# Performance work log

Measured on AMD Instinct MI355X. Metric: run time of the kernel, lower is better.

## Reference

```python
import jax, jax.numpy as jnp
import numpy as np

B = 256        # number of trees
L0 = 4096      # leaves per tree
L1 = 256       # layer-1 nodes per tree
D = 128        # input_dim == hidden_dim
OUT = 32       # output classes
EPS = 1e-5
N0 = B * L0    # 1,048,576 total leaves
N1 = B * L1    # 65,536 layer-1 nodes
N2 = B         # one root per tree


def _bn(x, g, b):
    # training-mode BatchNorm1d: biased variance over the node axis
    m = jnp.mean(x, axis=0)
    v = jnp.mean((x - m) ** 2, axis=0)
    return g * (x - m) * jax.lax.rsqrt(v + EPS) + b


def _mlp(h, w1, b1, g, beta, w2, b2):
    # GIN-style 2-layer MLP: relu(bn(linear)) -> linear
    return jax.nn.relu(_bn(h @ w1 + b1, g, beta)) @ w2 + b2


def setup_inputs() -> dict:
    key = jax.random.key(0)
    ks = jax.random.split(key, 16)

    def lin(k, fin, fout):
        kw, kb = jax.random.split(k)
        s = 1.0 / np.sqrt(fin)
        return (jax.random.uniform(kw, (fin, fout), jnp.float32, -s, s),
                jax.random.uniform(kb, (fout,), jnp.float32, -s, s))

    x = jax.random.normal(ks[0], (N0, D), jnp.float32)
    # structured tree indices: contiguous children per parent, contiguous trees
    parent1 = jnp.arange(N0, dtype=jnp.int64) // (L0 // L1)   # leaf -> layer1 parent (global)
    parent2 = jnp.arange(N1, dtype=jnp.int64) // L1           # layer1 -> root (global)
    tree0 = jnp.arange(N0, dtype=jnp.int64) // L0             # leaf -> tree id
    tree1 = jnp.arange(N1, dtype=jnp.int64) // L1             # layer1 node -> tree id

    m1w1, m1b1 = lin(ks[1], D, D)
    m1w2, m1b2 = lin(ks[2], D, D)
    m2w1, m2b1 = lin(ks[3], D, D)
    m2w2, m2b2 = lin(ks[4], D, D)
    wp, bp = lin(ks[5], D + 2 * D, OUT)

    ones = jnp.ones((D,), jnp.float32)
    zeros = jnp.zeros((D,), jnp.float32)
    return {
        "x": x, "parent1": parent1, "parent2": parent2, "tree0": tree0, "tree1": tree1,
        "mlp1_w1": m1w1, "mlp1_b1": m1b1, "mlp1_g": ones, "mlp1_beta": zeros,
        "mlp1_w2": m1w2, "mlp1_b2": m1b2, "bn1_g": ones, "bn1_b": zeros,
        "mlp2_w1": m2w1, "mlp2_b1": m2b1, "mlp2_g": ones, "mlp2_beta": zeros,
        "mlp2_w2": m2w2, "mlp2_b2": m2b2, "bn2_g": ones, "bn2_b": zeros,
        "wp": wp, "bp": bp,
    }


def reference(x, parent1, parent2, tree0, tree1,
              mlp1_w1, mlp1_b1, mlp1_g, mlp1_beta, mlp1_w2, mlp1_b2, bn1_g, bn1_b,
              mlp2_w1, mlp2_b1, mlp2_g, mlp2_beta, mlp2_w2, mlp2_b2, bn2_g, bn2_b,
              wp, bp):
    # layer 1: sparse child-sum (spmm with all-ones tree adjacency == segment_sum)
    p1 = jax.ops.segment_sum(x, parent1, num_segments=N1)              # [N1, D]
    h1 = jax.nn.relu(_bn(_mlp(p1, mlp1_w1, mlp1_b1, mlp1_g, mlp1_beta, mlp1_w2, mlp1_b2), bn1_g, bn1_b))
    # layer 2 (roots)
    p2 = jax.ops.segment_sum(h1, parent2, num_segments=N2)             # [B, D]
    h2 = jax.nn.relu(_bn(_mlp(p2, mlp2_w1, mlp2_b1, mlp2_g, mlp2_beta, mlp2_w2, mlp2_b2), bn2_g, bn2_b))
    # tree sum-pooling of layers 0..depth-1; layer depth is already per-tree
    g0 = jax.ops.segment_sum(x, tree0, num_segments=B)                 # [B, D]
    g1 = jax.ops.segment_sum(h1, tree1, num_segments=B)                # [B, D]
    rep = jnp.concatenate([g0, g1, h2], axis=1)                        # [B, 3D]
    return jax.nn.softmax(rep @ wp + bp, axis=1)                       # [B, OUT]
```

## Files before the change

### kernel.cpp

```cpp
#include <hip/hip_runtime.h>
#include <math.h>

#define D      128
#define D4     32
#define NTREE  256
#define NL1    65536
#define EPSBN  1e-5f

#define SC_OFF 0L
#define SD_OFF 256L
#define G0_OFF 512L
#define P2_OFF 33280L
#define ZERO_CNT 66048
#define SA_OFF 66048L
#define SB_OFF 66304L
#define T2_OFF 66560L
#define PBA_OFF 99328L
#define PBB_OFF 361472L
#define T1_OFF 623616L
#define U_OFF  9012224L

#define FMA4(A_, S_, W_) { (A_).x = fmaf((S_),(W_).x,(A_).x); (A_).y = fmaf((S_),(W_).y,(A_).y); \
                           (A_).z = fmaf((S_),(W_).z,(A_).z); (A_).w = fmaf((S_),(W_).w,(A_).w); }
#define ADD4(A_, B_)     { (A_).x += (B_).x; (A_).y += (B_).y; (A_).z += (B_).z; (A_).w += (B_).w; }
#define SQ4(Q_, V_)      { (Q_).x = fmaf((V_).x,(V_).x,(Q_).x); (Q_).y = fmaf((V_).y,(V_).y,(Q_).y); \
                           (Q_).z = fmaf((V_).z,(V_).z,(Q_).z); (Q_).w = fmaf((V_).w,(V_).w,(Q_).w); }
#define F4Z              make_float4(0.f,0.f,0.f,0.f)

__global__ __launch_bounds__(256) void k_zero(float* __restrict__ ws) {
    int i = blockIdx.x * 256 + threadIdx.x;
    if (i < ZERO_CNT) ws[i] = 0.f;
}

__global__ __launch_bounds__(256) void k_fused1(const float* __restrict__ x,
        const float* __restrict__ w1, const float* __restrict__ b1,
        float* __restrict__ t1, float* __restrict__ g0, float* __restrict__ pbufA)
{
    __shared__ __align__(16) float tile[64][D];
    __shared__ __align__(16) float red[2][8][D];
    const int t = threadIdx.x, b = blockIdx.x;
    const int w  = t >> 6;
    const int ln = t & 63;
    const int lc = ln & 31;
    const float4* __restrict__ x4 = (const float4*)x;

    float4 gacc = F4Z;
    #pragma unroll
    for (int pp = 0; pp < 4; ++pp) {
        const int p0 = pp * 16 + w * 4;
        #pragma unroll
        for (int r = 0; r < 4; ++r) {
            const long prow = (long)b * 64 + p0 + r;
            const long base = prow * 512 + ln;
            float4 a = F4Z;
            #pragma unroll
            for (int j = 0; j < 8; ++j) {
                float4 v = x4[base + j * 64];
                ADD4(a, v)
            }
            float4 o;
            o.x = __shfl_xor(a.x, 32); o.y = __shfl_xor(a.y, 32);
            o.z = __shfl_xor(a.z, 32); o.w = __shfl_xor(a.w, 32);
            ADD4(a, o)
            if (ln < 32) {
                *(float4*)&tile[p0 + r][lc*4] = a;
                ADD4(gacc, a)
            }
        }
    }
    if (ln < 32) *(float4*)&red[0][w][lc*4] = gacc;
    __syncthreads();
    if (t < 32) {
        float4 G = F4Z;
        #pragma unroll
        for (int g = 0; g < 4; ++g) { float4 vg = *(const float4*)&red[0][g][t*4]; ADD4(G, vg) }
        const int tree = b >> 2;
        atomicAdd(&g0[tree*D + t*4+0], G.x); atomicAdd(&g0[tree*D + t*4+1], G.y);
        atomicAdd(&g0[tree*D + t*4+2], G.z); atomicAdd(&g0[tree*D + t*4+3], G.w);
    }

    const int tc = t & 31, rg = t >> 5;
    float4* __restrict__ tv = (float4*)t1;
    const long base = (long)b * 64;
    float4 acc[8];
    const float4 bb = ((const float4*)b1)[tc];
    #pragma unroll
    for (int r = 0; r < 8; ++r) acc[r] = bb;
    const float4* __restrict__ wv = (const float4*)w1;
    #pragma unroll 4
    for (int k4 = 0; k4 < 32; ++k4) {
        float4 wr0 = wv[(k4*4+0)*D4 + tc];
        float4 wr1 = wv[(k4*4+1)*D4 + tc];
        float4 wr2 = wv[(k4*4+2)*D4 + tc];
        float4 wr3 = wv[(k4*4+3)*D4 + tc];
        #pragma unroll
        for (int r = 0; r < 8; ++r) {
            float4 a4 = *(const float4*)&tile[rg*8 + r][k4*4];
            FMA4(acc[r], a4.x, wr0) FMA4(acc[r], a4.y, wr1)
            FMA4(acc[r], a4.z, wr2) FMA4(acc[r], a4.w, wr3)
        }
    }
    #pragma unroll
    for (int r = 0; r < 8; ++r) tv[(base + rg*8 + r) * D4 + tc] = acc[r];

    float4 s4 = F4Z, q4 = F4Z;
    #pragma unroll
    for (int r = 0; r < 8; ++r) { ADD4(s4, acc[r]) SQ4(q4, acc[r]) }
    __syncthreads();
    *(float4*)&red[0][rg][tc*4] = s4;
    *(float4*)&red[1][rg][tc*4] = q4;
    __syncthreads();
    if (t < 32) {
        float4 S = F4Z;
        #pragma unroll
        for (int g = 0; g < 8; ++g) { float4 vs = *(const float4*)&red[0][g][t*4]; ADD4(S, vs) }
        *(float4*)&pbufA[b*256 + t*4] = S;
    } else if (t < 64) {
        const int c = t - 32;
        float4 Q = F4Z;
        #pragma unroll
        for (int g = 0; g < 8; ++g) { float4 vq = *(const float4*)&red[1][g][c*4]; ADD4(Q, vq) }
        *(float4*)&pbufA[b*256 + 128 + c*4] = Q;
    }
}

__global__ __launch_bounds__(256) void k_statR(const float* __restrict__ pbuf,
                                               float* __restrict__ stats)
{
    __shared__ float red[8][32];
    const int t = threadIdx.x, b = blockIdx.x;
    const int c = b * 32 + (t & 31);
    const int g = t >> 5;
    float s = 0.f;
    #pragma unroll 8
    for (int r = g; r < 1024; r += 8) s += pbuf[r*256 + c];
    red[g][t & 31] = s;
    __syncthreads();
    if (t < 32) {
        float S = 0.f;
        #pragma unroll
        for (int gg = 0; gg < 8; ++gg) S += red[gg][t];
        stats[b*32 + t] = S;
    }
}

__global__ __launch_bounds__(256) void k_mm2(const float* __restrict__ t1,
        const float* __restrict__ w2, const float* __restrict__ b2,
        const float* __restrict__ mg, const float* __restrict__ mbe,
        const float* __restrict__ statsA, float* __restrict__ u,
        float* __restrict__ pbufB)
{
    __shared__ __align__(16) float tile[64][D];
    __shared__ __align__(16) float red[2][8][D];
    const int t = threadIdx.x, b = blockIdx.x;
    const int tc = t & 31, rg = t >> 5;
    const float4* __restrict__ tv = (const float4*)t1;
    float4* __restrict__ uv = (float4*)u;
    const long base = (long)b * 64;

    float4 scv, shv;
    {
        const float inv = 1.f / (float)NL1;
        #pragma unroll
        for (int i = 0; i < 4; ++i) {
            const int c = tc*4 + i;
            float m  = statsA[c] * inv;
            float vv = statsA[D + c] * inv - m * m;
            float rs = rsqrtf(vv + EPSBN);
            float sc = mg[c] * rs;
            ((float*)&scv)[i] = sc;
            ((float*)&shv)[i] = mbe[c] - m * sc;
        }
    }
    #pragma unroll
    for (int i = 0; i < 8; ++i) {
        const int row = i * 8 + rg;
        float4 v = tv[(base + row) * D4 + tc];
        float4 y;
        y.x = fmaxf(fmaf(v.x, scv.x, shv.x), 0.f);
        y.y = fmaxf(fmaf(v.y, scv.y, shv.y), 0.f);
        y.z = fmaxf(fmaf(v.z, scv.z, shv.z), 0.f);
        y.w = fmaxf(fmaf(v.w, scv.w, shv.w), 0.f);
        *(float4*)&tile[row][tc*4] = y;
    }
    __syncthreads();

    float4 acc[8];
    const float4 bb = ((const float4*)b2)[tc];
    #pragma unroll
    for (int r = 0; r < 8; ++r) acc[r] = bb;
    const float4* __restrict__ wv = (const float4*)w2;
    #pragma unroll 4
    for (int k4 = 0; k4 < 32; ++k4) {
        float4 wr0 = wv[(k4*4+0)*D4 + tc];
        float4 wr1 = wv[(k4*4+1)*D4 + tc];
        float4 wr2 = wv[(k4*4+2)*D4 + tc];
        float4 wr3 = wv[(k4*4+3)*D4 + tc];
        #pragma unroll
        for (int r = 0; r < 8; ++r) {
            float4 a4 = *(const float4*)&tile[rg*8 + r][k4*4];
            FMA4(acc[r], a4.x, wr0) FMA4(acc[r], a4.y, wr1)
            FMA4(acc[r], a4.z, wr2) FMA4(acc[r], a4.w, wr3)
        }
    }
    #pragma unroll
    for (int r = 0; r < 8; ++r) uv[(base + rg*8 + r) * D4 + tc] = acc[r];

    float4 s4 = F4Z, q4 = F4Z;
    #pragma unroll
    for (int r = 0; r < 8; ++r) { ADD4(s4, acc[r]) SQ4(q4, acc[r]) }
    __syncthreads();
    *(float4*)&red[0][rg][tc*4] = s4;
    *(float4*)&red[1][rg][tc*4] = q4;
    __syncthreads();
    if (t < 32) {
        float4 S = F4Z;
        #pragma unroll
        for (int g = 0; g < 8; ++g) { float4 vs = *(const float4*)&red[0][g][t*4]; ADD4(S, vs) }
        *(float4*)&pbufB[b*256 + t*4] = S;
    } else if (t < 64) {
        const int c = t - 32;
        float4 Q = F4Z;
        #pragma unroll
        for (int g = 0; g < 8; ++g) { float4 vq = *(const float4*)&red[1][g][c*4]; ADD4(Q, vq) }
        *(float4*)&pbufB[b*256 + 128 + c*4] = Q;
    }
}

__global__ __launch_bounds__(256) void k_pool(const float* __restrict__ u,
        const float* __restrict__ bg, const float* __restrict__ bb_,
        const float* __restrict__ statsB, float* __restrict__ p2)
{
    __shared__ __align__(16) float red[8][D];
    const int t = threadIdx.x, b = blockIdx.x;
    const int tree = b >> 3, chunk = b & 7;
    const int tc = t & 31, rr = t >> 5;
    const float4* __restrict__ uv = (const float4*)u;

    float4 scv, shv;
    {
        const float inv = 1.f / (float)NL1;
        #pragma unroll
        for (int i = 0; i < 4; ++i) {
            const int c = tc*4 + i;
            float m  = statsB[c] * inv;
            float vv = statsB[D + c] * inv - m * m;
            float rs = rsqrtf(vv + EPSBN);
            float sc = bg[c] * rs;
            ((float*)&scv)[i] = sc;
            ((float*)&shv)[i] = bb_[c] - m * sc;
        }
    }
    const long rbase = (long)tree * 256 + chunk * 32;
    float4 ps = F4Z;
    #pragma unroll
    for (int i = 0; i < 4; ++i) {
        const int row = i * 8 + rr;
        float4 v = uv[(rbase + row) * D4 + tc];
        ps.x += fmaxf(fmaf(v.x, scv.x, shv.x), 0.f);
        ps.y += fmaxf(fmaf(v.y, scv.y, shv.y), 0.f);
        ps.z += fmaxf(fmaf(v.z, scv.z, shv.z), 0.f);
        ps.w += fmaxf(fmaf(v.w, scv.w, shv.w), 0.f);
    }
    *(float4*)&red[rr][tc*4] = ps;
    __syncthreads();
    if (t < 32) {
        float4 S = F4Z;
        #pragma unroll
        for (int g = 0; g < 8; ++g) { float4 vs = *(const float4*)&red[g][t*4]; ADD4(S, vs) }
        atomicAdd(&p2[tree*D + t*4+0], S.x); atomicAdd(&p2[tree*D + t*4+1], S.y);
        atomicAdd(&p2[tree*D + t*4+2], S.z); atomicAdd(&p2[tree*D + t*4+3], S.w);
    }
}

__global__ __launch_bounds__(256) void k_root1(const float* __restrict__ p2,
        const float* __restrict__ w1, const float* __restrict__ b1,
        float* __restrict__ t2, float* __restrict__ statsC)
{
    __shared__ __align__(16) float ps[8][D];
    __shared__ __align__(16) float red[2][8][D];
    const int t = threadIdx.x, b = blockIdx.x;
    const int j4 = t & 31, rr = t >> 5;
    *(float4*)&ps[rr][j4*4] = ((const float4*)p2)[(b*8 + rr)*D4 + j4];
    __syncthreads();
    const int row = t >> 5, tc = t & 31;
    const float4* wv = (const float4*)w1;
    float4 acc = ((const float4*)b1)[tc];
    #pragma unroll 8
    for (int k4 = 0; k4 < 32; ++k4) {
        float4 a = *(const float4*)&ps[row][k4*4];
        float4 wr0 = wv[(k4*4+0)*D4 + tc];
        float4 wr1 = wv[(k4*4+1)*D4 + tc];
        float4 wr2 = wv[(k4*4+2)*D4 + tc];
        float4 wr3 = wv[(k4*4+3)*D4 + tc];
        FMA4(acc, a.x, wr0) FMA4(acc, a.y, wr1) FMA4(acc, a.z, wr2) FMA4(acc, a.w, wr3)
    }
    ((float4*)t2)[(b*8 + row)*D4 + tc] = acc;
    float4 q;
    q.x = acc.x*acc.x; q.y = acc.y*acc.y; q.z = acc.z*acc.z; q.w = acc.w*acc.w;
    *(float4*)&red[0][row][tc*4] = acc;
    *(float4*)&red[1][row][tc*4] = q;
    __syncthreads();
    if (t < D) {
        float S = 0.f, Q = 0.f;
        #pragma unroll
        for (int g = 0; g < 8; ++g) { S += red[0][g][t]; Q += red[1][g][t]; }
        atomicAdd(&statsC[t], S);
        atomicAdd(&statsC[D+t], Q);
    }
}

__global__ __launch_bounds__(256) void k_root2(float* __restrict__ t2,
        const float* __restrict__ mg, const float* __restrict__ mb,
        const float* __restrict__ statsC,
        const float* __restrict__ w2, const float* __restrict__ b2,
        float* __restrict__ statsD)
{
    __shared__ __align__(16) float ysr[8][D];
    __shared__ __align__(16) float red[2][8][D];
    __shared__ __align__(16) float scs[D], shs[D];
    const int t = threadIdx.x, b = blockIdx.x;
    if (t < D) {
        float m = statsC[t] * (1.f / 256.f);
        float v = statsC[D+t] * (1.f / 256.f) - m * m;
        float rs = rsqrtf(v + EPSBN);
        float sc = mg[t] * rs;
        scs[t] = sc;
        shs[t] = mb[t] - m * sc;
    }
    __syncthreads();
    const int j4 = t & 31, rr = t >> 5;
    {
        float4 uu = ((const float4*)t2)[(b*8 + rr)*D4 + j4];
        float4 sc4 = *(const float4*)&scs[j4*4];
        float4 sh4 = *(const float4*)&shs[j4*4];
        float4 y;
        y.x = fmaxf(fmaf(uu.x, sc4.x, sh4.x), 0.f);
        y.y = fmaxf(fmaf(uu.y, sc4.y, sh4.y), 0.f);
        y.z = fmaxf(fmaf(uu.z, sc4.z, sh4.z), 0.f);
        y.w = fmaxf(fmaf(uu.w, sc4.w, sh4.w), 0.f);
        *(float4*)&ysr[rr][j4*4] = y;
    }
    __syncthreads();
    const int row = t >> 5, tc = t & 31;
    const float4* wv = (const float4*)w2;
    float4 acc = ((const float4*)b2)[tc];
    #pragma unroll 8
    for (int k4 = 0; k4 < 32; ++k4) {
        float4 a = *(const float4*)&ysr[row][k4*4];
        float4 wr0 = wv[(k4*4+0)*D4 + tc];
        float4 wr1 = wv[(k4*4+1)*D4 + tc];
        float4 wr2 = wv[(k4*4+2)*D4 + tc];
        float4 wr3 = wv[(k4*4+3)*D4 + tc];
        FMA4(acc, a.x, wr0) FMA4(acc, a.y, wr1) FMA4(acc, a.z, wr2) FMA4(acc, a.w, wr3)
    }
    ((float4*)t2)[(b*8 + row)*D4 + tc] = acc;
    float4 q;
    q.x = acc.x*acc.x; q.y = acc.y*acc.y; q.z = acc.z*acc.z; q.w = acc.w*acc.w;
    *(float4*)&red[0][row][tc*4] = acc;
    *(float4*)&red[1][row][tc*4] = q;
    __syncthreads();
    if (t < D) {
        float S = 0.f, Q = 0.f;
        #pragma unroll
        for (int g = 0; g < 8; ++g) { S += red[0][g][t]; Q += red[1][g][t]; }
        atomicAdd(&statsD[t], S);
        atomicAdd(&statsD[D+t], Q);
    }
}

__global__ __launch_bounds__(128) void k_final(const float* __restrict__ u2,
        const float* __restrict__ statsD,
        const float* __restrict__ bg, const float* __restrict__ bb_,
        const float* __restrict__ g0, const float* __restrict__ p2,
        const float* __restrict__ wp, const float* __restrict__ bp,
        float* __restrict__ out)
{
    __shared__ __align__(16) float reps[3*D];
    const int t = threadIdx.x, tree = blockIdx.x;
    if (t < D) {
        float m = statsD[t] * (1.f / 256.f);
        float v = statsD[D+t] * (1.f / 256.f) - m * m;
        float rs = rsqrtf(v + EPSBN);
        float sc = bg[t] * rs;
        float sh = bb_[t] - m * sc;
        reps[2*D + t] = fmaxf(fmaf(u2[tree*D + t], sc, sh), 0.f);
        reps[t]       = g0[tree*D + t];
        reps[D + t]   = p2[tree*D + t];
    }
    __syncthreads();
    if (t < 32) {
        float acc = bp[t];
        #pragma unroll 8
        for (int j = 0; j < 3*D; ++j) acc = fmaf(reps[j], wp[j*32 + t], acc);
        float mx = acc;
        #pragma unroll
        for (int mk = 16; mk > 0; mk >>= 1) mx = fmaxf(mx, __shfl_xor(mx, mk));
        float e = expf(acc - mx);
        float s = e;
        #pragma unroll
        for (int mk = 16; mk > 0; mk >>= 1) s += __shfl_xor(s, mk);
        out[tree*32 + t] = e / s;
    }
}

extern "C" void kernel_launch(void* const* d_in, const int* in_sizes, int n_in,
                              void* d_out, int out_size, void* d_ws, size_t ws_size,
                              hipStream_t stream)
{
    const float* x    = (const float*)d_in[0];
    const float* m1w1 = (const float*)d_in[5];
    const float* m1b1 = (const float*)d_in[6];
    const float* m1g  = (const float*)d_in[7];
    const float* m1be = (const float*)d_in[8];
    const float* m1w2 = (const float*)d_in[9];
    const float* m1b2 = (const float*)d_in[10];
    const float* bn1g = (const float*)d_in[11];
    const float* bn1b = (const float*)d_in[12];
    const float* m2w1 = (const float*)d_in[13];
    const float* m2b1 = (const float*)d_in[14];
    const float* m2g  = (const float*)d_in[15];
    const float* m2be = (const float*)d_in[16];
    const float* m2w2 = (const float*)d_in[17];
    const float* m2b2 = (const float*)d_in[18];
    const float* bn2g = (const float*)d_in[19];
    const float* bn2b = (const float*)d_in[20];
    const float* wp   = (const float*)d_in[21];
    const float* bp   = (const float*)d_in[22];
    float* out = (float*)d_out;
    float* ws  = (float*)d_ws;

    float* sC  = ws + SC_OFF;
    float* sD  = ws + SD_OFF;
    float* g0  = ws + G0_OFF;
    float* p2  = ws + P2_OFF;
    float* sA  = ws + SA_OFF;
    float* sB  = ws + SB_OFF;
    float* t2  = ws + T2_OFF;
    float* pbA = ws + PBA_OFF;
    float* pbB = ws + PBB_OFF;
    float* t1  = ws + T1_OFF;
    float* u   = ws + U_OFF;

    hipLaunchKernelGGL(k_zero,   dim3(258),  dim3(256), 0, stream, ws);
    hipLaunchKernelGGL(k_fused1, dim3(1024), dim3(256), 0, stream, x, m1w1, m1b1, t1, g0, pbA);
    hipLaunchKernelGGL(k_statR,  dim3(8),    dim3(256), 0, stream, pbA, sA);
    hipLaunchKernelGGL(k_mm2,    dim3(1024), dim3(256), 0, stream, t1, m1w2, m1b2, m1g, m1be, sA, u, pbB);
    hipLaunchKernelGGL(k_statR,  dim3(8),    dim3(256), 0, stream, pbB, sB);
    hipLaunchKernelGGL(k_pool,   dim3(2048), dim3(256), 0, stream, u, bn1g, bn1b, sB, p2);
    hipLaunchKernelGGL(k_root1,  dim3(32),   dim3(256), 0, stream, p2, m2w1, m2b1, t2, sC);
    hipLaunchKernelGGL(k_root2,  dim3(32),   dim3(256), 0, stream, t2, m2g, m2be, sC, m2w2, m2b2, sD);
    hipLaunchKernelGGL(k_final,  dim3(256),  dim3(128), 0, stream, t2, sD, bn2g, bn2b, g0, p2, wp, bp, out);
}
```

Baseline: 246.2 us.

## Replace global atomics and zeroing kernel with deterministic partial-buffer reductions

```diff
diff --git a/kernel.cpp b/kernel.cpp
--- a/kernel.cpp
+++ b/kernel.cpp
@@ -7,18 +7,18 @@
 #define NL1    65536
 #define EPSBN  1e-5f
 
-#define SC_OFF 0L
-#define SD_OFF 256L
-#define G0_OFF 512L
-#define P2_OFF 33280L
-#define ZERO_CNT 66048
-#define SA_OFF 66048L
-#define SB_OFF 66304L
-#define T2_OFF 66560L
-#define PBA_OFF 99328L
-#define PBB_OFF 361472L
-#define T1_OFF 623616L
-#define U_OFF  9012224L
+#define SA_OFF   0L
+#define SB_OFF   256L
+#define G0_OFF   512L
+#define P2_OFF   33280L
+#define T2_OFF   66048L
+#define SCP_OFF  98816L
+#define SDP_OFF  107008L
+#define PBP_OFF  115200L
+#define PBA_OFF  377344L
+#define PBB_OFF  1163776L
+#define T1_OFF   1425920L
+#define U_OFF    9814528L
 
 #define FMA4(A_, S_, W_) { (A_).x = fmaf((S_),(W_).x,(A_).x); (A_).y = fmaf((S_),(W_).y,(A_).y); \
                            (A_).z = fmaf((S_),(W_).z,(A_).z); (A_).w = fmaf((S_),(W_).w,(A_).w); }
@@ -27,17 +27,11 @@
                            (Q_).z = fmaf((V_).z,(V_).z,(Q_).z); (Q_).w = fmaf((V_).w,(V_).w,(Q_).w); }
 #define F4Z              make_float4(0.f,0.f,0.f,0.f)
 
-__global__ __launch_bounds__(256) void k_zero(float* __restrict__ ws) {
-    int i = blockIdx.x * 256 + threadIdx.x;
-    if (i < ZERO_CNT) ws[i] = 0.f;
-}
-
 __global__ __launch_bounds__(256) void k_fused1(const float* __restrict__ x,
         const float* __restrict__ w1, const float* __restrict__ b1,
-        float* __restrict__ t1, float* __restrict__ g0, float* __restrict__ pbufA)
+        float* __restrict__ t1, float* __restrict__ pbufA)
 {
     __shared__ __align__(16) float tile[64][D];
-    __shared__ __align__(16) float red[2][8][D];
     const int t = threadIdx.x, b = blockIdx.x;
     const int w  = t >> 6;
     const int ln = t & 63;
@@ -68,16 +62,8 @@
             }
         }
     }
-    if (ln < 32) *(float4*)&red[0][w][lc*4] = gacc;
-    __syncthreads();
-    if (t < 32) {
-        float4 G = F4Z;
-        #pragma unroll
-        for (int g = 0; g < 4; ++g) { float4 vg = *(const float4*)&red[0][g][t*4]; ADD4(G, vg) }
-        const int tree = b >> 2;
-        atomicAdd(&g0[tree*D + t*4+0], G.x); atomicAdd(&g0[tree*D + t*4+1], G.y);
-        atomicAdd(&g0[tree*D + t*4+2], G.z); atomicAdd(&g0[tree*D + t*4+3], G.w);
-    }
+    if (ln < 32) *(float4*)&pbufA[(long)b*768 + 256 + w*128 + lc*4] = gacc;
+    __syncthreads();
 
     const int tc = t & 31, rg = t >> 5;
     float4* __restrict__ tv = (float4*)t1;
@@ -107,6 +93,7 @@
     #pragma unroll
     for (int r = 0; r < 8; ++r) { ADD4(s4, acc[r]) SQ4(q4, acc[r]) }
     __syncthreads();
+    float (*red)[8][D] = (float(*)[8][D])tile;
     *(float4*)&red[0][rg][tc*4] = s4;
     *(float4*)&red[1][rg][tc*4] = q4;
     __syncthreads();
@@ -114,18 +101,51 @@
         float4 S = F4Z;
         #pragma unroll
         for (int g = 0; g < 8; ++g) { float4 vs = *(const float4*)&red[0][g][t*4]; ADD4(S, vs) }
-        *(float4*)&pbufA[b*256 + t*4] = S;
+        *(float4*)&pbufA[(long)b*768 + t*4] = S;
     } else if (t < 64) {
         const int c = t - 32;
         float4 Q = F4Z;
         #pragma unroll
         for (int g = 0; g < 8; ++g) { float4 vq = *(const float4*)&red[1][g][c*4]; ADD4(Q, vq) }
-        *(float4*)&pbufA[b*256 + 128 + c*4] = Q;
-    }
-}
-
-__global__ __launch_bounds__(256) void k_statR(const float* __restrict__ pbuf,
-                                               float* __restrict__ stats)
+        *(float4*)&pbufA[(long)b*768 + 128 + c*4] = Q;
+    }
+}
+
+__global__ __launch_bounds__(256) void k_redA(const float* __restrict__ pbufA,
+        float* __restrict__ statsA, float* __restrict__ g0)
+{
+    const int t = threadIdx.x, b = blockIdx.x;
+    if (b < 8) {
+        __shared__ float red[8][32];
+        const int c = b * 32 + (t & 31);
+        const int g = t >> 5;
+        float s = 0.f;
+        #pragma unroll 8
+        for (int r = g; r < 1024; r += 8) s += pbufA[(long)r*768 + c];
+        red[g][t & 31] = s;
+        __syncthreads();
+        if (t < 32) {
+            float S = 0.f;
+            #pragma unroll
+            for (int gg = 0; gg < 8; ++gg) S += red[gg][t];
+            statsA[b*32 + t] = S;
+        }
+    } else {
+        const int idx = b - 8;
+        const int tree = idx * 2 + (t >> 7);
+        const int c = t & 127;
+        float s = 0.f;
+        #pragma unroll
+        for (int jb = 0; jb < 4; ++jb)
+            #pragma unroll
+            for (int wvi = 0; wvi < 4; ++wvi)
+                s += pbufA[(long)(tree*4 + jb)*768 + 256 + wvi*128 + c];
+        g0[tree*D + c] = s;
+    }
+}
+
+__global__ __launch_bounds__(256) void k_redB(const float* __restrict__ pbuf,
+                                              float* __restrict__ stats)
 {
     __shared__ float red[8][32];
     const int t = threadIdx.x, b = blockIdx.x;
@@ -151,7 +171,6 @@
         float* __restrict__ pbufB)
 {
     __shared__ __align__(16) float tile[64][D];
-    __shared__ __align__(16) float red[2][8][D];
     const int t = threadIdx.x, b = blockIdx.x;
     const int tc = t & 31, rg = t >> 5;
     const float4* __restrict__ tv = (const float4*)t1;
@@ -210,6 +229,7 @@
     #pragma unroll
     for (int r = 0; r < 8; ++r) { ADD4(s4, acc[r]) SQ4(q4, acc[r]) }
     __syncthreads();
+    float (*red)[8][D] = (float(*)[8][D])tile;
     *(float4*)&red[0][rg][tc*4] = s4;
     *(float4*)&red[1][rg][tc*4] = q4;
     __syncthreads();
@@ -229,7 +249,7 @@
 
 __global__ __launch_bounds__(256) void k_pool(const float* __restrict__ u,
         const float* __restrict__ bg, const float* __restrict__ bb_,
-        const float* __restrict__ statsB, float* __restrict__ p2)
+        const float* __restrict__ statsB, float* __restrict__ pbufP)
 {
     __shared__ __align__(16) float red[8][D];
     const int t = threadIdx.x, b = blockIdx.x;
@@ -268,20 +288,29 @@
         float4 S = F4Z;
         #pragma unroll
         for (int g = 0; g < 8; ++g) { float4 vs = *(const float4*)&red[g][t*4]; ADD4(S, vs) }
-        atomicAdd(&p2[tree*D + t*4+0], S.x); atomicAdd(&p2[tree*D + t*4+1], S.y);
-        atomicAdd(&p2[tree*D + t*4+2], S.z); atomicAdd(&p2[tree*D + t*4+3], S.w);
-    }
-}
-
-__global__ __launch_bounds__(256) void k_root1(const float* __restrict__ p2,
+        *(float4*)&pbufP[(long)b*D + t*4] = S;
+    }
+}
+
+__global__ __launch_bounds__(256) void k_root1(const float* __restrict__ pbufP,
         const float* __restrict__ w1, const float* __restrict__ b1,
-        float* __restrict__ t2, float* __restrict__ statsC)
+        float* __restrict__ p2, float* __restrict__ t2, float* __restrict__ sCp)
 {
     __shared__ __align__(16) float ps[8][D];
     __shared__ __align__(16) float red[2][8][D];
     const int t = threadIdx.x, b = blockIdx.x;
     const int j4 = t & 31, rr = t >> 5;
-    *(float4*)&ps[rr][j4*4] = ((const float4*)p2)[(b*8 + rr)*D4 + j4];
+    {
+        const int tree = b*8 + rr;
+        float4 S = F4Z;
+        #pragma unroll
+        for (int ch = 0; ch < 8; ++ch) {
+            float4 v = *(const float4*)&pbufP[(long)(tree*8 + ch)*D + j4*4];
+            ADD4(S, v)
+        }
+        *(float4*)&ps[rr][j4*4] = S;
+        ((float4*)p2)[tree*D4 + j4] = S;
+    }
     __syncthreads();
     const int row = t >> 5, tc = t & 31;
     const float4* wv = (const float4*)w1;
@@ -305,24 +334,27 @@
         float S = 0.f, Q = 0.f;
         #pragma unroll
         for (int g = 0; g < 8; ++g) { S += red[0][g][t]; Q += red[1][g][t]; }
-        atomicAdd(&statsC[t], S);
-        atomicAdd(&statsC[D+t], Q);
+        sCp[b*256 + t]     = S;
+        sCp[b*256 + D + t] = Q;
     }
 }
 
 __global__ __launch_bounds__(256) void k_root2(float* __restrict__ t2,
         const float* __restrict__ mg, const float* __restrict__ mb,
-        const float* __restrict__ statsC,
+        const float* __restrict__ sCp,
         const float* __restrict__ w2, const float* __restrict__ b2,
-        float* __restrict__ statsD)
+        float* __restrict__ sDp)
 {
     __shared__ __align__(16) float ysr[8][D];
     __shared__ __align__(16) float red[2][8][D];
     __shared__ __align__(16) float scs[D], shs[D];
     const int t = threadIdx.x, b = blockIdx.x;
     if (t < D) {
-        float m = statsC[t] * (1.f / 256.f);
-        float v = statsC[D+t] * (1.f / 256.f) - m * m;
+        float S = 0.f, Q = 0.f;
+        #pragma unroll 8
+        for (int j = 0; j < 32; ++j) { S += sCp[j*256 + t]; Q += sCp[j*256 + D + t]; }
+        float m = S * (1.f / 256.f);
+        float v = Q * (1.f / 256.f) - m * m;
         float rs = rsqrtf(v + EPSBN);
         float sc = mg[t] * rs;
         scs[t] = sc;
@@ -364,13 +396,13 @@
         float S = 0.f, Q = 0.f;
         #pragma unroll
         for (int g = 0; g < 8; ++g) { S += red[0][g][t]; Q += red[1][g][t]; }
-        atomicAdd(&statsD[t], S);
-        atomicAdd(&statsD[D+t], Q);
+        sDp[b*256 + t]     = S;
+        sDp[b*256 + D + t] = Q;
     }
 }
 
 __global__ __launch_bounds__(128) void k_final(const float* __restrict__ u2,
-        const float* __restrict__ statsD,
+        const float* __restrict__ sDp,
         const float* __restrict__ bg, const float* __restrict__ bb_,
         const float* __restrict__ g0, const float* __restrict__ p2,
         const float* __restrict__ wp, const float* __restrict__ bp,
@@ -379,8 +411,11 @@
     __shared__ __align__(16) float reps[3*D];
     const int t = threadIdx.x, tree = blockIdx.x;
     if (t < D) {
-        float m = statsD[t] * (1.f / 256.f);
-        float v = statsD[D+t] * (1.f / 256.f) - m * m;
+        float S = 0.f, Q = 0.f;
+        #pragma unroll 8
+        for (int j = 0; j < 32; ++j) { S += sDp[j*256 + t]; Q += sDp[j*256 + D + t]; }
+        float m = S * (1.f / 256.f);
+        float v = Q * (1.f / 256.f) - m * m;
         float rs = rsqrtf(v + EPSBN);
         float sc = bg[t] * rs;
         float sh = bb_[t] - m * sc;
@@ -430,25 +465,25 @@
     float* out = (float*)d_out;
     float* ws  = (float*)d_ws;
 
-    float* sC  = ws + SC_OFF;
-    float* sD  = ws + SD_OFF;
-    float* g0  = ws + G0_OFF;
-    float* p2  = ws + P2_OFF;
-    float* sA  = ws + SA_OFF;
-    float* sB  = ws + SB_OFF;
-    float* t2  = ws + T2_OFF;
-    float* pbA = ws + PBA_OFF;
-    float* pbB = ws + PBB_OFF;
-    float* t1  = ws + T1_OFF;
-    float* u   = ws + U_OFF;
-
-    hipLaunchKernelGGL(k_zero,   dim3(258),  dim3(256), 0, stream, ws);
-    hipLaunchKernelGGL(k_fused1, dim3(1024), dim3(256), 0, stream, x, m1w1, m1b1, t1, g0, pbA);
-    hipLaunchKernelGGL(k_statR,  dim3(8),    dim3(256), 0, stream, pbA, sA);
+    float* sA   = ws + SA_OFF;
+    float* sB   = ws + SB_OFF;
+    float* g0   = ws + G0_OFF;
+    float* p2   = ws + P2_OFF;
+    float* t2   = ws + T2_OFF;
+    float* sCp  = ws + SCP_OFF;
+    float* sDp  = ws + SDP_OFF;
+    float* pbP  = ws + PBP_OFF;
+    float* pbA  = ws + PBA_OFF;
+    float* pbB  = ws + PBB_OFF;
+    float* t1   = ws + T1_OFF;
+    float* u    = ws + U_OFF;
+
+    hipLaunchKernelGGL(k_fused1, dim3(1024), dim3(256), 0, stream, x, m1w1, m1b1, t1, pbA);
+    hipLaunchKernelGGL(k_redA,   dim3(136),  dim3(256), 0, stream, pbA, sA, g0);
     hipLaunchKernelGGL(k_mm2,    dim3(1024), dim3(256), 0, stream, t1, m1w2, m1b2, m1g, m1be, sA, u, pbB);
-    hipLaunchKernelGGL(k_statR,  dim3(8),    dim3(256), 0, stream, pbB, sB);
-    hipLaunchKernelGGL(k_pool,   dim3(2048), dim3(256), 0, stream, u, bn1g, bn1b, sB, p2);
-    hipLaunchKernelGGL(k_root1,  dim3(32),   dim3(256), 0, stream, p2, m2w1, m2b1, t2, sC);
-    hipLaunchKernelGGL(k_root2,  dim3(32),   dim3(256), 0, stream, t2, m2g, m2be, sC, m2w2, m2b2, sD);
-    hipLaunchKernelGGL(k_final,  dim3(256),  dim3(128), 0, stream, t2, sD, bn2g, bn2b, g0, p2, wp, bp, out);
-}
+    hipLaunchKernelGGL(k_redB,   dim3(8),    dim3(256), 0, stream, pbB, sB);
+    hipLaunchKernelGGL(k_pool,   dim3(2048), dim3(256), 0, stream, u, bn1g, bn1b, sB, pbP);
+    hipLaunchKernelGGL(k_root1,  dim3(32),   dim3(256), 0, stream, pbP, m2w1, m2b1, p2, t2, sCp);
+    hipLaunchKernelGGL(k_root2,  dim3(32),   dim3(256), 0, stream, t2, m2g, m2be, sCp, m2w2, m2b2, sDp);
+    hipLaunchKernelGGL(k_final,  dim3(256),  dim3(128), 0, stream, t2, sDp, bn2g, bn2b, g0, p2, wp, bp, out);
+}
```

New measurement: 265.1 us. +7.6%, slower.
